# Kernel optimization log

Hardware: AMD Instinct MI355X
Metric: run time of the kernel (lower is better)

Reference implementation:

```python
import jax, jax.numpy as jnp
import numpy as np

B, S, A, MSG, C = 524288, 64, 16, 32, 4
CH = 9 + S  # children_states feature dim = 73
EPS = 1e-12  # F.normalize clamp_min eps


def _l2norm(v):
    n = jnp.sqrt(jnp.sum(v * v, axis=-1, keepdims=True))
    return v / jnp.maximum(n, EPS)


def setup_inputs() -> dict:
    key = jax.random.key(0)
    ks = jax.random.split(key, 12)
    def lin(kw, kb, out_d, in_d):
        bound = 1.0 / np.sqrt(in_d)
        W = jax.random.uniform(kw, (out_d, in_d), minval=-bound, maxval=bound, dtype=jnp.float32)
        b = jax.random.uniform(kb, (out_d,), minval=-bound, maxval=bound, dtype=jnp.float32)
        return W, b
    W1, b1 = lin(ks[0], ks[1], 64, S + A)
    W2, b2 = lin(ks[2], ks[3], 64, 64 + MSG)
    W3, b3 = lin(ks[4], ks[5], MSG, 64)
    Wa, ba = lin(ks[6], ks[7], MSG, CH)
    return {
        "x": jax.random.normal(ks[8], (B, S), dtype=jnp.float32),
        "u": jax.random.normal(ks[9], (B, A), dtype=jnp.float32),
        "children_states": jax.random.normal(ks[10], (B, C, CH), dtype=jnp.float32),
        "m": jax.random.normal(ks[11], (B, C * MSG), dtype=jnp.float32),
        "W1": W1, "b1": b1, "W2": W2, "b2": b2, "W3": W3, "b3": b3,
        "Wa": Wa, "ba": ba,
    }


def reference(x, u, children_states, m, W1, b1, W2, b2, W3, b3, Wa, ba):
    # fc1 on cat(x, u), then L2 normalize
    xu = jnp.concatenate([x, u], axis=-1) @ W1.T + b1          # [B, 64]
    xu = _l2norm(xu)
    # attention over children (softmax along child axis, dim=-2)
    att = jax.nn.softmax(children_states @ Wa.T + ba, axis=-2)  # [B, C, MSG]
    mm = m.reshape(*children_states.shape[:-1], -1)             # [B, C, MSG]
    magg = jnp.sum(mm * att, axis=-2)                           # [B, MSG]
    # fused MLP tail
    xum = jnp.tanh(jnp.concatenate([xu, magg], axis=-1))        # [B, 64+MSG]
    xum = jnp.tanh(xum @ W2.T + b2)                             # [B, 64]
    xum = xum @ W3.T + b3                                       # [B, MSG]
    return _l2norm(xum)
```

## Files before the change

### kernel.cpp

```cpp
#include <hip/hip_runtime.h>
#include <cstddef>

typedef __fp16 f16x8 __attribute__((ext_vector_type(8)));
typedef float f32x4 __attribute__((ext_vector_type(4)));
typedef unsigned int uint32;
typedef unsigned short ushort;

constexpr int S = 64, MSG = 32, CH = 73;

constexpr int FC1_OFF = 0;
constexpr int ATT_OFF = 12 * 512;
constexpr int FC2_OFF = 18 * 512;
constexpr int FC3_OFF = 30 * 512;
constexpr int WS_ELEMS = 34 * 512;

__global__ void prep_pack(const float* __restrict__ W1, const float* __restrict__ b1,
                          const float* __restrict__ Wa, const float* __restrict__ ba,
                          const float* __restrict__ W2, const float* __restrict__ W3,
                          ushort* __restrict__ wsf) {
  int idx = blockIdx.x * 256 + threadIdx.x;
  if (idx >= WS_ELEMS) return;
  int tile = idx >> 9;
  int lane = (idx >> 3) & 63;
  int e = idx & 7;
  int jloc = lane & 15;
  int kloc = ((lane >> 4) << 3) + e;
  float v = 0.f;
  if (tile < 12) {
    int t = tile >> 2, f = tile & 3;
    int j = f * 16 + jloc, k = t * 32 + kloc;
    v = (k < 80) ? W1[j * 80 + k] : (k == 80 ? b1[j] : 0.f);
  } else if (tile < 18) {
    int q = tile - 12, t = q >> 1, f = q & 1;
    int j = f * 16 + jloc, k = t * 32 + kloc;
    v = (k < 73) ? Wa[j * 73 + k] : (k == 73 ? ba[j] : 0.f);
  } else if (tile < 30) {
    int q = tile - 18, t = q >> 2, f = q & 3;
    int j = f * 16 + jloc, k = t * 32 + kloc;
    v = W2[j * 96 + k];
  } else {
    int q = tile - 30, t = q >> 1, f = q & 1;
    int j = f * 16 + jloc, k = t * 32 + kloc;
    v = W3[j * 64 + k];
  }
  union { __fp16 h; ushort s; } cv;
  cv.h = (__fp16)v;
  wsf[idx] = cv.s;
}

__device__ __forceinline__ f32x4 mf(f16x8 a, f16x8 b, f32x4 c) {
  return __builtin_amdgcn_mfma_f32_16x16x32_f16(a, b, c, 0, 0, 0);
}
__device__ __forceinline__ uint32 pku(float a, float b) {
  auto r = __builtin_amdgcn_cvt_pkrtz(a, b);
  union { decltype(r) f; uint32 u; } v; v.f = r; return v.u;
}
__device__ __forceinline__ f16x8 packA(const float* f) {
  union { uint32 u[4]; f16x8 h; } r;
  r.u[0] = pku(f[0], f[1]); r.u[1] = pku(f[2], f[3]);
  r.u[2] = pku(f[4], f[5]); r.u[3] = pku(f[6], f[7]);
  return r.h;
}
__device__ __forceinline__ f16x8 packA2(float4 a, float4 b) {
  union { uint32 u[4]; f16x8 h; } r;
  r.u[0] = pku(a.x, a.y); r.u[1] = pku(a.z, a.w);
  r.u[2] = pku(b.x, b.y); r.u[3] = pku(b.z, b.w);
  return r.h;
}
__device__ __forceinline__ float fast_tanh(float v) {
  v = fminf(15.f, fmaxf(-15.f, v));
  float t = __expf(2.f * v);
  return (t - 1.f) * __builtin_amdgcn_rcpf(t + 1.f);
}

constexpr int HT_LD = 104;
constexpr int H2_LD = 72;
constexpr int HBUF_B = 3328;
constexpr int UNION_OFF = 13312;
constexpr int UNION_B = 4672;
constexpr int SMEM_B = 32000;

__launch_bounds__(256)
__global__ void critic_mfma_kernel(
    const float* __restrict__ x, const float* __restrict__ u,
    const float* __restrict__ cs, const float* __restrict__ m,
    const float* __restrict__ b2, const float* __restrict__ b3,
    const ushort* __restrict__ wsf, float* __restrict__ out, int n) {
  __shared__ __attribute__((aligned(16))) unsigned char smem[SMEM_B];

  const int wave = threadIdx.x >> 6;
  const int lane = threadIdx.x & 63;
  const int lm = lane & 15;
  const int lq = lane >> 4;

  const int tiles = n >> 4;
  const int wslots = gridDim.x * 4;
  const int tbase = blockIdx.x * 4 + wave;
  if (tbase >= tiles) return;

  __fp16* __restrict__ ht = reinterpret_cast<__fp16*>(smem + wave * HBUF_B);
  float* __restrict__ csw = reinterpret_cast<float*>(smem + UNION_OFF + wave * UNION_B);
  __fp16* __restrict__ h2t = reinterpret_cast<__fp16*>(smem + UNION_OFF + wave * UNION_B);

  auto ldB = [&](int off_tile) -> f16x8 {
    return *reinterpret_cast<const f16x8*>(wsf + off_tile + lane * 8);
  };

  f16x8 wa[6];
#pragma unroll
  for (int i = 0; i < 6; ++i) wa[i] = ldB(ATT_OFF + i * 512);

  float4 csr0, csr1, csr2, csr3, csr4;
  float4 xva, xvb, xvc, xvd, uva, uvb;

  auto issue_cs = [&](int r0, int g) {
    const float4* __restrict__ src =
        reinterpret_cast<const float4*>(cs + (size_t)(r0 * 4 + 16 * g) * CH);
    csr0 = src[lane];       csr1 = src[64 + lane];
    csr2 = src[128 + lane]; csr3 = src[192 + lane];
    if (lane < 36) csr4 = src[256 + lane];
  };
  auto issue_xu = [&](int r0) {
    const float4* __restrict__ xrow4 =
        reinterpret_cast<const float4*>(x + (size_t)(r0 + lm) * S);
    xva = xrow4[2 * lq]; xvb = xrow4[2 * lq + 1];
    xvc = xrow4[8 + 2 * lq]; xvd = xrow4[9 + 2 * lq];
    const int uq = (lq < 2) ? lq : 0;
    const float4* __restrict__ urow4 =
        reinterpret_cast<const float4*>(u + (size_t)(r0 + lm) * 16);
    uva = urow4[2 * uq]; uvb = urow4[2 * uq + 1];
  };

  issue_cs(tbase << 4, 0);
  issue_xu(tbase << 4);

  for (int t = 0; t < 2; ++t) {
    const int tile = tbase + t * wslots;
    if (tile >= tiles) break;
    const int r0 = tile << 4;
    const int ntile = tile + wslots;
    const bool pre_next = (t == 0) && (ntile < tiles);

#pragma unroll
    for (int g = 0; g < 4; ++g) {
      {
        float4* __restrict__ dst = reinterpret_cast<float4*>(csw);
        dst[lane] = csr0;       dst[64 + lane] = csr1;
        dst[128 + lane] = csr2; dst[192 + lane] = csr3;
        if (lane < 36) dst[256 + lane] = csr4;
      }
      float mr[8];
      {
        const float* __restrict__ mrow = m + (size_t)(r0 + 4 * g + lq) * 128;
#pragma unroll
        for (int c = 0; c < 4; ++c) {
          mr[c * 2 + 0] = mrow[c * 32 + lm];
          mr[c * 2 + 1] = mrow[c * 32 + lm + 16];
        }
      }
      if (g < 3) issue_cs(r0, g + 1);
      else if (pre_next) issue_cs(ntile << 4, 0);

      const float* __restrict__ crow = csw + lm * CH;
      f32x4 zac[2] = {{0.f, 0.f, 0.f, 0.f}, {0.f, 0.f, 0.f, 0.f}};
#pragma unroll
      for (int tt = 0; tt < 3; ++tt) {
        float f[8];
        const int kbase = tt * 32 + lq * 8;
#pragma unroll
        for (int e = 0; e < 8; ++e) {
          int k = kbase + e;
          f[e] = (k < 73) ? crow[k] : (k == 73 ? 1.f : 0.f);
        }
        f16x8 af = packA(f);
        zac[0] = mf(af, wa[tt * 2 + 0], zac[0]);
        zac[1] = mf(af, wa[tt * 2 + 1], zac[1]);
      }
#pragma unroll
      for (int f = 0; f < 2; ++f) {
        const int j = lm + 16 * f;
        float e0 = __expf(zac[f][0]);
        float e1 = __expf(zac[f][1]);
        float e2 = __expf(zac[f][2]);
        float e3 = __expf(zac[f][3]);
        float den = (e0 + e1) + (e2 + e3);
        float num = fmaf(mr[0 * 2 + f], e0,
                    fmaf(mr[1 * 2 + f], e1,
                    fmaf(mr[2 * 2 + f], e2, mr[3 * 2 + f] * e3)));
        float mg = num * __builtin_amdgcn_rcpf(den);
        ht[(4 * g + lq) * HT_LD + 64 + j] = (__fp16)fast_tanh(mg);
      }
    }

    f32x4 hac[4] = {{0.f,0.f,0.f,0.f},{0.f,0.f,0.f,0.f},{0.f,0.f,0.f,0.f},{0.f,0.f,0.f,0.f}};
    {
      f16x8 a0 = packA2(xva, xvb);
      f16x8 a1 = packA2(xvc, xvd);
      float f[8];
      float uf[8] = {uva.x, uva.y, uva.z, uva.w, uvb.x, uvb.y, uvb.z, uvb.w};
#pragma unroll
      for (int e = 0; e < 8; ++e) {
        int k = 64 + lq * 8 + e;
        f[e] = (k < 80) ? ((lq < 2) ? uf[e] : 0.f) : (k == 80 ? 1.f : 0.f);
      }
      f16x8 a2f = packA(f);
      if (pre_next) issue_xu(ntile << 4);
#pragma unroll
      for (int fi = 0; fi < 4; ++fi) hac[fi] = mf(a0, ldB(FC1_OFF + fi * 512), hac[fi]);
#pragma unroll
      for (int fi = 0; fi < 4; ++fi) hac[fi] = mf(a1, ldB(FC1_OFF + (4 + fi) * 512), hac[fi]);
#pragma unroll
      for (int fi = 0; fi < 4; ++fi) hac[fi] = mf(a2f, ldB(FC1_OFF + (8 + fi) * 512), hac[fi]);
    }
    {
      float rn[4];
#pragma unroll
      for (int reg = 0; reg < 4; ++reg) {
        float s = hac[0][reg] * hac[0][reg];
        s = fmaf(hac[1][reg], hac[1][reg], s);
        s = fmaf(hac[2][reg], hac[2][reg], s);
        s = fmaf(hac[3][reg], hac[3][reg], s);
        s += __shfl_xor(s, 1);
        s += __shfl_xor(s, 2);
        s += __shfl_xor(s, 4);
        s += __shfl_xor(s, 8);
        rn[reg] = __builtin_amdgcn_rcpf(fmaxf(sqrtf(s), 1e-12f));
      }
#pragma unroll
      for (int fi = 0; fi < 4; ++fi)
#pragma unroll
        for (int reg = 0; reg < 4; ++reg)
          ht[(4 * lq + reg) * HT_LD + lm + 16 * fi] =
              (__fp16)fast_tanh(hac[fi][reg] * rn[reg]);
    }

    {
      f32x4 ac2[4] = {{0.f,0.f,0.f,0.f},{0.f,0.f,0.f,0.f},{0.f,0.f,0.f,0.f},{0.f,0.f,0.f,0.f}};
      f16x8 a2[3];
#pragma unroll
      for (int tt = 0; tt < 3; ++tt)
        a2[tt] = *reinterpret_cast<const f16x8*>(ht + lm * HT_LD + tt * 32 + lq * 8);
#pragma unroll
      for (int tt = 0; tt < 3; ++tt)
#pragma unroll
        for (int fi = 0; fi < 4; ++fi)
          ac2[fi] = mf(a2[tt], ldB(FC2_OFF + (tt * 4 + fi) * 512), ac2[fi]);
#pragma unroll
      for (int fi = 0; fi < 4; ++fi) {
        float bv = b2[lm + 16 * fi];
#pragma unroll
        for (int reg = 0; reg < 4; ++reg)
          h2t[(4 * lq + reg) * H2_LD + lm + 16 * fi] =
              (__fp16)fast_tanh(ac2[fi][reg] + bv);
      }
    }

    {
      f32x4 o[2] = {{0.f,0.f,0.f,0.f},{0.f,0.f,0.f,0.f}};
      f16x8 a3[2];
#pragma unroll
      for (int tt = 0; tt < 2; ++tt)
        a3[tt] = *reinterpret_cast<const f16x8*>(h2t + lm * H2_LD + tt * 32 + lq * 8);
#pragma unroll
      for (int tt = 0; tt < 2; ++tt)
#pragma unroll
        for (int fi = 0; fi < 2; ++fi)
          o[fi] = mf(a3[tt], ldB(FC3_OFF + (tt * 2 + fi) * 512), o[fi]);
#pragma unroll
      for (int fi = 0; fi < 2; ++fi) {
        float bv = b3[lm + 16 * fi];
#pragma unroll
        for (int reg = 0; reg < 4; ++reg) o[fi][reg] += bv;
      }
      float rn2[4];
#pragma unroll
      for (int reg = 0; reg < 4; ++reg) {
        float s = fmaf(o[0][reg], o[0][reg], o[1][reg] * o[1][reg]);
        s += __shfl_xor(s, 1);
        s += __shfl_xor(s, 2);
        s += __shfl_xor(s, 4);
        s += __shfl_xor(s, 8);
        rn2[reg] = __builtin_amdgcn_rcpf(fmaxf(sqrtf(s), 1e-12f));
      }
#pragma unroll
      for (int fi = 0; fi < 2; ++fi)
#pragma unroll
        for (int reg = 0; reg < 4; ++reg)
          out[(size_t)(r0 + 4 * lq + reg) * MSG + lm + 16 * fi] =
              o[fi][reg] * rn2[reg];
    }
  }
}

extern "C" void kernel_launch(void* const* d_in, const int* in_sizes, int n_in,
                              void* d_out, int out_size, void* d_ws, size_t ws_size,
                              hipStream_t stream) {
  const float* x  = (const float*)d_in[0];
  const float* u  = (const float*)d_in[1];
  const float* cs = (const float*)d_in[2];
  const float* m  = (const float*)d_in[3];
  const float* W1 = (const float*)d_in[4];
  const float* b1 = (const float*)d_in[5];
  const float* W2 = (const float*)d_in[6];
  const float* b2 = (const float*)d_in[7];
  const float* W3 = (const float*)d_in[8];
  const float* b3 = (const float*)d_in[9];
  const float* Wa = (const float*)d_in[10];
  const float* ba = (const float*)d_in[11];
  float* out = (float*)d_out;
  ushort* wsf = (ushort*)d_ws;

  const int n = in_sizes[0] / S;
  const int tiles = (n + 15) / 16;

  hipLaunchKernelGGL(prep_pack, dim3((WS_ELEMS + 255) / 256), dim3(256), 0, stream,
                     W1, b1, Wa, ba, W2, W3, wsf);

  const int blocks = (tiles + 7) / 8;
  hipLaunchKernelGGL(critic_mfma_kernel, dim3(blocks), dim3(256), 0, stream,
                     x, u, cs, m, b2, b3, wsf, out, n);
}
```

Before: 230.8 us.

## Double-buffer children_states and m loads two groups ahead in attention loop

Replaces the single set of children_states prefetch registers with two alternating register sets (A/B), so each group's load is issued two groups ahead instead of one. The m-row loads are also prefetched one group ahead into ping-pong arrays rather than loaded on demand. The goal is to hide more global-memory latency behind the MFMA and softmax work. The cost is roughly twenty extra VGPRs per lane, which may lower occupancy.

```diff
diff --git a/kernel.cpp b/kernel.cpp
--- a/kernel.cpp
+++ b/kernel.cpp
@@ -110,17 +110,45 @@
 #pragma unroll
   for (int i = 0; i < 6; ++i) wa[i] = ldB(ATT_OFF + i * 512);
 
-  float4 csr0, csr1, csr2, csr3, csr4;
+  float4 A0, A1, A2, A3, A4, B0, B1, B2, B3, B4;
+  float MA[8], MB[8];
   float4 xva, xvb, xvc, xvd, uva, uvb;
 
-  auto issue_cs = [&](int r0, int g) {
+  auto issueCsA = [&](int row16) {
     const float4* __restrict__ src =
-        reinterpret_cast<const float4*>(cs + (size_t)(r0 * 4 + 16 * g) * CH);
-    csr0 = src[lane];       csr1 = src[64 + lane];
-    csr2 = src[128 + lane]; csr3 = src[192 + lane];
-    if (lane < 36) csr4 = src[256 + lane];
-  };
-  auto issue_xu = [&](int r0) {
+        reinterpret_cast<const float4*>(cs + (size_t)row16 * CH);
+    A0 = src[lane];       A1 = src[64 + lane];
+    A2 = src[128 + lane]; A3 = src[192 + lane];
+    if (lane < 36) A4 = src[256 + lane];
+  };
+  auto issueCsB = [&](int row16) {
+    const float4* __restrict__ src =
+        reinterpret_cast<const float4*>(cs + (size_t)row16 * CH);
+    B0 = src[lane];       B1 = src[64 + lane];
+    B2 = src[128 + lane]; B3 = src[192 + lane];
+    if (lane < 36) B4 = src[256 + lane];
+  };
+  auto commitA = [&]() {
+    float4* __restrict__ dst = reinterpret_cast<float4*>(csw);
+    dst[lane] = A0;       dst[64 + lane] = A1;
+    dst[128 + lane] = A2; dst[192 + lane] = A3;
+    if (lane < 36) dst[256 + lane] = A4;
+  };
+  auto commitB = [&]() {
+    float4* __restrict__ dst = reinterpret_cast<float4*>(csw);
+    dst[lane] = B0;       dst[64 + lane] = B1;
+    dst[128 + lane] = B2; dst[192 + lane] = B3;
+    if (lane < 36) dst[256 + lane] = B4;
+  };
+  auto issueM = [&](float* MR, int r0, int g) {
+    const float* __restrict__ mrow = m + (size_t)(r0 + 4 * g + lq) * 128;
+#pragma unroll
+    for (int c = 0; c < 4; ++c) {
+      MR[c * 2 + 0] = mrow[c * 32 + lm];
+      MR[c * 2 + 1] = mrow[c * 32 + lm + 16];
+    }
+  };
+  auto issueXU = [&](int r0) {
     const float4* __restrict__ xrow4 =
         reinterpret_cast<const float4*>(x + (size_t)(r0 + lm) * S);
     xva = xrow4[2 * lq]; xvb = xrow4[2 * lq + 1];
@@ -131,65 +159,66 @@
     uva = urow4[2 * uq]; uvb = urow4[2 * uq + 1];
   };
 
-  issue_cs(tbase << 4, 0);
-  issue_xu(tbase << 4);
+  auto attnBody = [&](int r0, int g, const float* MR) {
+    const float* __restrict__ crow = csw + lm * CH;
+    f32x4 zac[2] = {{0.f, 0.f, 0.f, 0.f}, {0.f, 0.f, 0.f, 0.f}};
+#pragma unroll
+    for (int tt = 0; tt < 3; ++tt) {
+      float f[8];
+      const int kbase = tt * 32 + lq * 8;
+#pragma unroll
+      for (int e = 0; e < 8; ++e) {
+        int k = kbase + e;
+        f[e] = (k < 73) ? crow[k] : (k == 73 ? 1.f : 0.f);
+      }
+      f16x8 af = packA(f);
+      zac[0] = mf(af, wa[tt * 2 + 0], zac[0]);
+      zac[1] = mf(af, wa[tt * 2 + 1], zac[1]);
+    }
+#pragma unroll
+    for (int f = 0; f < 2; ++f) {
+      const int j = lm + 16 * f;
+      float e0 = __expf(zac[f][0]);
+      float e1 = __expf(zac[f][1]);
+      float e2 = __expf(zac[f][2]);
+      float e3 = __expf(zac[f][3]);
+      float den = (e0 + e1) + (e2 + e3);
+      float num = fmaf(MR[0 + f], e0,
+                  fmaf(MR[2 + f], e1,
+                  fmaf(MR[4 + f], e2, MR[6 + f] * e3)));
+      float mg = num * __builtin_amdgcn_rcpf(den);
+      ht[(4 * g + lq) * HT_LD + 64 + j] = (__fp16)fast_tanh(mg);
+    }
+  };
+
+  const int r0_0 = tbase << 4;
+  const int ntile = tbase + wslots;
+  const bool has2 = ntile < tiles;
+  const int r0_1 = has2 ? (ntile << 4) : r0_0;
+
+  issueCsA(r0_0 * 4);
+  issueM(MA, r0_0, 0);
+  issueCsB(r0_0 * 4 + 16);
+  issueXU(r0_0);
 
   for (int t = 0; t < 2; ++t) {
-    const int tile = tbase + t * wslots;
-    if (tile >= tiles) break;
-    const int r0 = tile << 4;
-    const int ntile = tile + wslots;
-    const bool pre_next = (t == 0) && (ntile < tiles);
+    if (t == 1 && !has2) break;
+    const int r0 = t ? r0_1 : r0_0;
+    const bool pn = (t == 0) && has2;
 
 #pragma unroll
     for (int g = 0; g < 4; ++g) {
-      {
-        float4* __restrict__ dst = reinterpret_cast<float4*>(csw);
-        dst[lane] = csr0;       dst[64 + lane] = csr1;
-        dst[128 + lane] = csr2; dst[192 + lane] = csr3;
-        if (lane < 36) dst[256 + lane] = csr4;
-      }
-      float mr[8];
-      {
-        const float* __restrict__ mrow = m + (size_t)(r0 + 4 * g + lq) * 128;
-#pragma unroll
-        for (int c = 0; c < 4; ++c) {
-          mr[c * 2 + 0] = mrow[c * 32 + lm];
-          mr[c * 2 + 1] = mrow[c * 32 + lm + 16];
-        }
-      }
-      if (g < 3) issue_cs(r0, g + 1);
-      else if (pre_next) issue_cs(ntile << 4, 0);
-
-      const float* __restrict__ crow = csw + lm * CH;
-      f32x4 zac[2] = {{0.f, 0.f, 0.f, 0.f}, {0.f, 0.f, 0.f, 0.f}};
-#pragma unroll
-      for (int tt = 0; tt < 3; ++tt) {
-        float f[8];
-        const int kbase = tt * 32 + lq * 8;
-#pragma unroll
-        for (int e = 0; e < 8; ++e) {
-          int k = kbase + e;
-          f[e] = (k < 73) ? crow[k] : (k == 73 ? 1.f : 0.f);
-        }
-        f16x8 af = packA(f);
-        zac[0] = mf(af, wa[tt * 2 + 0], zac[0]);
-        zac[1] = mf(af, wa[tt * 2 + 1], zac[1]);
-      }
-#pragma unroll
-      for (int f = 0; f < 2; ++f) {
-        const int j = lm + 16 * f;
-        float e0 = __expf(zac[f][0]);
-        float e1 = __expf(zac[f][1]);
-        float e2 = __expf(zac[f][2]);
-        float e3 = __expf(zac[f][3]);
-        float den = (e0 + e1) + (e2 + e3);
-        float num = fmaf(mr[0 * 2 + f], e0,
-                    fmaf(mr[1 * 2 + f], e1,
-                    fmaf(mr[2 * 2 + f], e2, mr[3 * 2 + f] * e3)));
-        float mg = num * __builtin_amdgcn_rcpf(den);
-        ht[(4 * g + lq) * HT_LD + 64 + j] = (__fp16)fast_tanh(mg);
-      }
+      if ((g & 1) == 0) commitA(); else commitB();
+      if (g < 2) {
+        if ((g & 1) == 0) issueCsA(r0 * 4 + 16 * (g + 2));
+        else              issueCsB(r0 * 4 + 16 * (g + 2));
+      } else if (pn) {
+        if ((g & 1) == 0) issueCsA(r0_1 * 4 + 16 * (g - 2));
+        else              issueCsB(r0_1 * 4 + 16 * (g - 2));
+      }
+      if (g < 3)      issueM(((g & 1) == 0) ? MB : MA, r0, g + 1);
+      else if (pn)    issueM(MA, r0_1, 0);
+      attnBody(r0, g, ((g & 1) == 0) ? MA : MB);
     }
 
     f32x4 hac[4] = {{0.f,0.f,0.f,0.f},{0.f,0.f,0.f,0.f},{0.f,0.f,0.f,0.f},{0.f,0.f,0.f,0.f}};
@@ -204,7 +233,7 @@
         f[e] = (k < 80) ? ((lq < 2) ? uf[e] : 0.f) : (k == 80 ? 1.f : 0.f);
       }
       f16x8 a2f = packA(f);
-      if (pre_next) issue_xu(ntile << 4);
+      if (pn) issueXU(r0_1);
 #pragma unroll
       for (int fi = 0; fi < 4; ++fi) hac[fi] = mf(a0, ldB(FC1_OFF + fi * 512), hac[fi]);
 #pragma unroll
```

Measured after the change: 263.3 us. 1.14x slower.
